# Kernel tuning notes

Hardware: AMD Instinct MI355X
Metric: run time of the kernel (lower is better)

The kernel has to match this reference:

```python
import jax, jax.numpy as jnp
import numpy as np

N, E, G, D = 100000, 400000, 4000, 128
AF, BF, L = 74, 12, 11  # atom/bond feat sizes; L = n_layers-1 GNN layers after GetContext


def _p(k, shape, fan):
    return jax.random.normal(k, shape, dtype=jnp.float32) * (fan ** -0.5)


def setup_inputs() -> dict:
    key = jax.random.key(0)
    ks = iter(jax.random.split(key, 32))
    z = lambda *s: jnp.zeros(s, jnp.float32)
    return dict(
        atom_feats=jax.random.normal(next(ks), (N, AF), jnp.float32),
        bond_feats=jax.random.normal(next(ks), (E, BF), jnp.float32),
        src=jax.random.randint(next(ks), (E,), 0, N, jnp.int32),
        dst=jax.random.randint(next(ks), (E,), 0, N, jnp.int32),
        node_graph_ids=jnp.sort(jax.random.randint(next(ks), (N,), 0, G, jnp.int32)),
        W_node=_p(next(ks), (AF, D), AF), b_node=z(D),
        W_edge1=_p(next(ks), (AF + BF, D), AF + BF), b_edge1=z(D),
        W_edge2=_p(next(ks), (2 * D, 1), 2 * D), b_edge2=z(1),
        W_et=_p(next(ks), (D, D), D), b_et=z(D),
        gru0_Wih=_p(next(ks), (3 * D, D), D), gru0_bih=z(3 * D),
        gru0_Whh=_p(next(ks), (3 * D, D), D), gru0_bhh=z(3 * D),
        Wpe=_p(next(ks), (L, 2 * D, 1), 2 * D), bpe=z(L, 1),
        Wpn=_p(next(ks), (L, D, D), D), bpn=z(L, D),
        gru_Wih=_p(next(ks), (L, 3 * D, D), D), gru_bih=z(L, 3 * D),
        gru_Whh=_p(next(ks), (L, 3 * D, D), D), gru_bhh=z(L, 3 * D),
        Wr1=_p(next(ks), (D, D), D), br1=z(D),
        Wr2=_p(next(ks), (D, D), D), br2=z(D),
    )


def leaky_relu(x):
    return jnp.where(x > 0, x, 0.01 * x)


def edge_softmax(logits, dst):
    # softmax of edge logits grouped by destination node (DGL edge_softmax)
    m = jax.ops.segment_max(logits, dst, num_segments=N)
    m = jnp.where(jnp.isfinite(m), m, 0.0)
    e = jnp.exp(logits - m[dst])
    s = jax.ops.segment_sum(e, dst, num_segments=N)
    return e / s[dst]


def gru_cell(x, h, Wih, bih, Whh, bhh):
    gi = x @ Wih.T + bih
    gh = h @ Whh.T + bhh
    ir, iz, ig = jnp.split(gi, 3, axis=-1)
    hr, hz, hg = jnp.split(gh, 3, axis=-1)
    r = jax.nn.sigmoid(ir + hr)
    z = jax.nn.sigmoid(iz + hz)
    n = jnp.tanh(ig + r * hg)
    return (1.0 - z) * n + z * h


def _attentive_fp(atom_feats, bond_feats, src, dst, node_graph_ids,
                  W_node, b_node, W_edge1, b_edge1, W_edge2, b_edge2,
                  W_et, b_et, gru0_Wih, gru0_bih, gru0_Whh, gru0_bhh,
                  Wpe, bpe, Wpn, bpn, gru_Wih, gru_bih, gru_Whh, gru_bhh,
                  Wr1, br1, Wr2, br2):
    # --- GetContext (dropout = identity at inference) ---
    hv_new = leaky_relu(atom_feats @ W_node + b_node)                       # [N,D]
    he1 = leaky_relu(jnp.concatenate([atom_feats[src], bond_feats], 1) @ W_edge1 + b_edge1)  # [E,D]
    logits = leaky_relu(jnp.concatenate([hv_new[dst], he1], 1) @ W_edge2 + b_edge2)          # [E,1]
    a = edge_softmax(logits, dst)
    c = jax.ops.segment_sum(a * (he1 @ W_et + b_et), dst, num_segments=N)   # [N,D]
    h = jax.nn.relu(gru_cell(jax.nn.elu(c), hv_new, gru0_Wih, gru0_bih, gru0_Whh, gru0_bhh))

    # --- 11 GNNLayers (AttentiveGRU2) via scan over stacked params ---
    def layer(h, p):
        Wpe_l, bpe_l, Wpn_l, bpn_l, Wih, bih, Whh, bhh = p
        lg = leaky_relu(jnp.concatenate([h[dst], h[src]], 1) @ Wpe_l + bpe_l)  # [E,1]
        a = edge_softmax(lg, dst)
        hp = h @ Wpn_l + bpn_l
        c = jax.ops.segment_sum(hp[src] * a, dst, num_segments=N)
        return jax.nn.relu(gru_cell(jax.nn.elu(c), h, Wih, bih, Whh, bhh)), None

    h, _ = jax.lax.scan(layer, h, (Wpe, bpe, Wpn, bpn, gru_Wih, gru_bih, gru_Whh, gru_bhh))

    # --- MLPNodeReadout, mode='mean' ---
    x = jax.nn.relu(h @ Wr1 + br1) @ Wr2 + br2
    sums = jax.ops.segment_sum(x, node_graph_ids, num_segments=G)
    counts = jax.ops.segment_sum(jnp.ones((N, 1), x.dtype), node_graph_ids, num_segments=G)
    return sums / jnp.maximum(counts, 1.0)                                  # [G,D]


def reference(atom_feats, bond_feats, src, dst, node_graph_ids,
              W_node, b_node, W_edge1, b_edge1, W_edge2, b_edge2,
              W_et, b_et, gru0_Wih, gru0_bih, gru0_Whh, gru0_bhh,
              Wpe, bpe, Wpn, bpn, gru_Wih, gru_bih, gru_Whh, gru_bhh,
              Wr1, br1, Wr2, br2):
    return _attentive_fp(atom_feats, bond_feats, src, dst, node_graph_ids,
                         W_node, b_node, W_edge1, b_edge1, W_edge2, b_edge2,
                         W_et, b_et, gru0_Wih, gru0_bih, gru0_Whh, gru0_bhh,
                         Wpe, bpe, Wpn, bpn, gru_Wih, gru_bih, gru_Whh, gru_bhh,
                         Wr1, br1, Wr2, br2)
```

## Files before the change

### kernel.cpp

```cpp
#include <hip/hip_runtime.h>
#include <cstdio>
#include <cstddef>

enum { ACT_NONE = 0, ACT_LEAKY = 1, ACT_RELU = 2 };

typedef __attribute__((ext_vector_type(8))) short short8v;
typedef __attribute__((ext_vector_type(4))) float f32x4;

__device__ __forceinline__ float leakyf(float x) { return x > 0.f ? x : 0.01f * x; }

__device__ __forceinline__ unsigned fenc(float f) {
    unsigned u = __float_as_uint(f);
    return (u & 0x80000000u) ? ~u : (u | 0x80000000u);
}
__device__ __forceinline__ float fdec(unsigned u) {
    return (u & 0x80000000u) ? __uint_as_float(u & 0x7FFFFFFFu) : __uint_as_float(~u);
}

__device__ __forceinline__ unsigned bf16rtn(float x) {
    unsigned u = __float_as_uint(x);
    return (u + 0x7FFFu + ((u >> 16) & 1u)) >> 16;
}
__device__ __forceinline__ void split8(float4 a, float4 b, short8v& hi, short8v& lo) {
    const float v[8] = {a.x, a.y, a.z, a.w, b.x, b.y, b.z, b.w};
#pragma unroll
    for (int i = 0; i < 8; i++) {
        const unsigned hb = bf16rtn(v[i]);
        const float r = v[i] - __uint_as_float(hb << 16);
        hi[i] = (short)hb;
        lo[i] = (short)bf16rtn(r);
    }
}

__global__ __launch_bounds__(256) void wsplit_k(
    const float* __restrict__ Wih, const float* __restrict__ Whh,
    unsigned short* __restrict__ whi, unsigned short* __restrict__ wlo)
{
    const int i4 = (blockIdx.x * 256 + threadIdx.x) * 4;
    if (i4 >= 98304) return;
    const float* src = (i4 < 49152) ? (Wih + i4) : (Whh + (i4 - 49152));
    const float4 v = *(const float4*)src;
    const float vv[4] = {v.x, v.y, v.z, v.w};
    unsigned short h4[4], l4[4];
#pragma unroll
    for (int i = 0; i < 4; i++) {
        const unsigned hb = bf16rtn(vv[i]);
        const float r = vv[i] - __uint_as_float(hb << 16);
        h4[i] = (unsigned short)hb;
        l4[i] = (unsigned short)bf16rtn(r);
    }
    *(ushort4*)&whi[i4] = make_ushort4(h4[0], h4[1], h4[2], h4[3]);
    *(ushort4*)&wlo[i4] = make_ushort4(l4[0], l4[1], l4[2], l4[3]);
}

__global__ __launch_bounds__(256) void wsplitT_k(
    const float* __restrict__ W,
    unsigned short* __restrict__ whi, unsigned short* __restrict__ wlo)
{
    const int idx = blockIdx.x * 256 + threadIdx.x;
    if (idx >= 16384) return;
    const int k = idx >> 7, col = idx & 127;
    const float v = W[idx];
    const unsigned hb = bf16rtn(v);
    const float r = v - __uint_as_float(hb << 16);
    whi[col * 128 + k] = (unsigned short)hb;
    wlo[col * 128 + k] = (unsigned short)bf16rtn(r);
}

__global__ __launch_bounds__(256) void wsplitT96_k(
    const float* __restrict__ W,
    unsigned short* __restrict__ whi, unsigned short* __restrict__ wlo, int K)
{
    const int idx = blockIdx.x * 256 + threadIdx.x;
    if (idx >= 12288) return;
    const int col = idx / 96, k = idx - col * 96;
    const float v = (k < K) ? W[(size_t)k * 128 + col] : 0.f;
    const unsigned hb = bf16rtn(v);
    const float r = v - __uint_as_float(hb << 16);
    whi[idx] = (unsigned short)hb;
    wlo[idx] = (unsigned short)bf16rtn(r);
}

__global__ __launch_bounds__(512) void gru_fused_mfma_k(
    const float* __restrict__ cbuf, const unsigned short* __restrict__ whi,
    const unsigned short* __restrict__ wlo, const float* __restrict__ bih,
    const float* __restrict__ bhh, float* __restrict__ h, int M)
{
    __shared__ short lhi[4][4][64][8];
    __shared__ short llo[4][4][64][8];
    const int t    = threadIdx.x;
    const int lane = t & 63;
    const int w    = t >> 6;
    const int rBase = blockIdx.x * 64;

    const int sRS = t >> 3, sQ = t & 7;
    const int sRow = rBase + sRS;
    const int sRT = sRS >> 4, sLrow = sRS & 15;

    auto stage = [&](const float* __restrict__ A, bool doElu) {
#pragma unroll
        for (int half = 0; half < 2; half++) {
            const int k0 = sQ * 16 + half * 8;
            const int kc = k0 >> 5;
            const int g  = (k0 & 31) >> 3;
            float4 f0 = make_float4(0.f, 0.f, 0.f, 0.f);
            float4 f1 = make_float4(0.f, 0.f, 0.f, 0.f);
            if (sRow < M) {
                f0 = *(const float4*)&A[(size_t)sRow * 128 + k0];
                f1 = *(const float4*)&A[(size_t)sRow * 128 + k0 + 4];
                if (doElu) {
                    f0.x = f0.x > 0.f ? f0.x : expm1f(f0.x);
                    f0.y = f0.y > 0.f ? f0.y : expm1f(f0.y);
                    f0.z = f0.z > 0.f ? f0.z : expm1f(f0.z);
                    f0.w = f0.w > 0.f ? f0.w : expm1f(f0.w);
                    f1.x = f1.x > 0.f ? f1.x : expm1f(f1.x);
                    f1.y = f1.y > 0.f ? f1.y : expm1f(f1.y);
                    f1.z = f1.z > 0.f ? f1.z : expm1f(f1.z);
                    f1.w = f1.w > 0.f ? f1.w : expm1f(f1.w);
                }
            }
            short8v h8, l8;
            split8(f0, f1, h8, l8);
            *(short8v*)&lhi[sRT][kc][sLrow + g * 16][0] = h8;
            *(short8v*)&llo[sRT][kc][sLrow + g * 16][0] = l8;
        }
    };

    f32x4 accr[4], accz[4], accig[4], acchg[4];
#pragma unroll
    for (int rt = 0; rt < 4; rt++) {
        accr[rt]  = (f32x4){0.f, 0.f, 0.f, 0.f};
        accz[rt]  = (f32x4){0.f, 0.f, 0.f, 0.f};
        accig[rt] = (f32x4){0.f, 0.f, 0.f, 0.f};
        acchg[rt] = (f32x4){0.f, 0.f, 0.f, 0.f};
    }

    const int cw   = w * 16 + (lane & 15);
    const int koff = (lane >> 4) * 8;

    stage(cbuf, true);
    __syncthreads();
#pragma unroll
    for (int kc = 0; kc < 4; kc++) {
        short8v bh[3], bl[3];
#pragma unroll
        for (int g = 0; g < 3; g++) {
            const size_t off = (size_t)(g * 128 + cw) * 128 + kc * 32 + koff;
            bh[g] = *(const short8v*)&whi[off];
            bl[g] = *(const short8v*)&wlo[off];
        }
#pragma unroll
        for (int rt = 0; rt < 4; rt++) {
            const short8v ah = *(const short8v*)&lhi[rt][kc][lane][0];
            const short8v al = *(const short8v*)&llo[rt][kc][lane][0];
            accr[rt]  = __builtin_amdgcn_mfma_f32_16x16x32_bf16(ah, bh[0], accr[rt], 0, 0, 0);
            accr[rt]  = __builtin_amdgcn_mfma_f32_16x16x32_bf16(al, bh[0], accr[rt], 0, 0, 0);
            accr[rt]  = __builtin_amdgcn_mfma_f32_16x16x32_bf16(ah, bl[0], accr[rt], 0, 0, 0);
            accz[rt]  = __builtin_amdgcn_mfma_f32_16x16x32_bf16(ah, bh[1], accz[rt], 0, 0, 0);
            accz[rt]  = __builtin_amdgcn_mfma_f32_16x16x32_bf16(al, bh[1], accz[rt], 0, 0, 0);
            accz[rt]  = __builtin_amdgcn_mfma_f32_16x16x32_bf16(ah, bl[1], accz[rt], 0, 0, 0);
            accig[rt] = __builtin_amdgcn_mfma_f32_16x16x32_bf16(ah, bh[2], accig[rt], 0, 0, 0);
            accig[rt] = __builtin_amdgcn_mfma_f32_16x16x32_bf16(al, bh[2], accig[rt], 0, 0, 0);
            accig[rt] = __builtin_amdgcn_mfma_f32_16x16x32_bf16(ah, bl[2], accig[rt], 0, 0, 0);
        }
    }
    __syncthreads();

    stage(h, false);
    __syncthreads();
#pragma unroll
    for (int kc = 0; kc < 4; kc++) {
        short8v bh[3], bl[3];
#pragma unroll
        for (int g = 0; g < 3; g++) {
            const size_t off = (size_t)(384 + g * 128 + cw) * 128 + kc * 32 + koff;
            bh[g] = *(const short8v*)&whi[off];
            bl[g] = *(const short8v*)&wlo[off];
        }
#pragma unroll
        for (int rt = 0; rt < 4; rt++) {
            const short8v ah = *(const short8v*)&lhi[rt][kc][lane][0];
            const short8v al = *(const short8v*)&llo[rt][kc][lane][0];
            accr[rt]  = __builtin_amdgcn_mfma_f32_16x16x32_bf16(ah, bh[0], accr[rt], 0, 0, 0);
            accr[rt]  = __builtin_amdgcn_mfma_f32_16x16x32_bf16(al, bh[0], accr[rt], 0, 0, 0);
            accr[rt]  = __builtin_amdgcn_mfma_f32_16x16x32_bf16(ah, bl[0], accr[rt], 0, 0, 0);
            accz[rt]  = __builtin_amdgcn_mfma_f32_16x16x32_bf16(ah, bh[1], accz[rt], 0, 0, 0);
            accz[rt]  = __builtin_amdgcn_mfma_f32_16x16x32_bf16(al, bh[1], accz[rt], 0, 0, 0);
            accz[rt]  = __builtin_amdgcn_mfma_f32_16x16x32_bf16(ah, bl[1], accz[rt], 0, 0, 0);
            acchg[rt] = __builtin_amdgcn_mfma_f32_16x16x32_bf16(ah, bh[2], acchg[rt], 0, 0, 0);
            acchg[rt] = __builtin_amdgcn_mfma_f32_16x16x32_bf16(al, bh[2], acchg[rt], 0, 0, 0);
            acchg[rt] = __builtin_amdgcn_mfma_f32_16x16x32_bf16(ah, bl[2], acchg[rt], 0, 0, 0);
        }
    }

    const float br_  = bih[cw] + bhh[cw];
    const float bz_  = bih[128 + cw] + bhh[128 + cw];
    const float big_ = bih[256 + cw];
    const float bhg_ = bhh[256 + cw];
#pragma unroll
    for (int rt = 0; rt < 4; rt++) {
        const int r0 = rBase + rt * 16 + ((lane >> 4) << 2);
#pragma unroll
        for (int i = 0; i < 4; i++) {
            const int row = r0 + i;
            if (row >= M) continue;
            const float hv = h[(size_t)row * 128 + cw];
            const float r  = 1.f / (1.f + expf(-(accr[rt][i] + br_)));
            const float z  = 1.f / (1.f + expf(-(accz[rt][i] + bz_)));
            const float nn = tanhf(accig[rt][i] + big_ + r * (acchg[rt][i] + bhg_));
            h[(size_t)row * 128 + cw] = fmaxf((1.f - z) * nn + z * hv, 0.f);
        }
    }
}

__global__ __launch_bounds__(512) void mfma128_k(
    const float* __restrict__ A, const unsigned short* __restrict__ whi,
    const unsigned short* __restrict__ wlo, const float* __restrict__ bias,
    float* __restrict__ C, int M, int actOut)
{
    __shared__ short lhi[4][4][64][8];
    __shared__ short llo[4][4][64][8];
    const int t    = threadIdx.x;
    const int lane = t & 63;
    const int w    = t >> 6;
    const int rBase = blockIdx.x * 64;

    {
        const int rS = t >> 3, q = t & 7;
        const int row = rBase + rS;
        const int rt = rS >> 4, lrow = rS & 15;
#pragma unroll
        for (int half = 0; half < 2; half++) {
            const int k0 = q * 16 + half * 8;
            const int kc = k0 >> 5;
            const int g  = (k0 & 31) >> 3;
            float4 f0 = make_float4(0.f, 0.f, 0.f, 0.f);
            float4 f1 = make_float4(0.f, 0.f, 0.f, 0.f);
            if (row < M) {
                f0 = *(const float4*)&A[(size_t)row * 128 + k0];
                f1 = *(const float4*)&A[(size_t)row * 128 + k0 + 4];
            }
            short8v h8, l8;
            split8(f0, f1, h8, l8);
            *(short8v*)&lhi[rt][kc][lrow + g * 16][0] = h8;
            *(short8v*)&llo[rt][kc][lrow + g * 16][0] = l8;
        }
    }
    __syncthreads();

    f32x4 acc[4];
#pragma unroll
    for (int rt = 0; rt < 4; rt++) acc[rt] = (f32x4){0.f, 0.f, 0.f, 0.f};

    const int cw   = w * 16 + (lane & 15);
    const int koff = (lane >> 4) * 8;

#pragma unroll
    for (int kc = 0; kc < 4; kc++) {
        const size_t off = (size_t)cw * 128 + kc * 32 + koff;
        const short8v bh = *(const short8v*)&whi[off];
        const short8v bl = *(const short8v*)&wlo[off];
#pragma unroll
        for (int rt = 0; rt < 4; rt++) {
            const short8v ah = *(const short8v*)&lhi[rt][kc][lane][0];
            const short8v al = *(const short8v*)&llo[rt][kc][lane][0];
            acc[rt] = __builtin_amdgcn_mfma_f32_16x16x32_bf16(ah, bh, acc[rt], 0, 0, 0);
            acc[rt] = __builtin_amdgcn_mfma_f32_16x16x32_bf16(al, bh, acc[rt], 0, 0, 0);
            acc[rt] = __builtin_amdgcn_mfma_f32_16x16x32_bf16(ah, bl, acc[rt], 0, 0, 0);
        }
    }

    const float b0 = bias[cw];
#pragma unroll
    for (int rt = 0; rt < 4; rt++) {
        const int r0 = rBase + rt * 16 + ((lane >> 4) << 2);
#pragma unroll
        for (int i = 0; i < 4; i++) {
            const int row = r0 + i;
            if (row >= M) continue;
            float v = acc[rt][i] + b0;
            if (actOut == ACT_LEAKY)      v = v > 0.f ? v : 0.01f * v;
            else if (actOut == ACT_RELU)  v = fmaxf(v, 0.f);
            C[(size_t)row * 128 + cw] = v;
        }
    }
}

__global__ __launch_bounds__(512) void mfma96_k(
    const float* __restrict__ A1, const float* __restrict__ A2,
    const int* __restrict__ idx,
    const unsigned short* __restrict__ whi, const unsigned short* __restrict__ wlo,
    const float* __restrict__ bias, float* __restrict__ C,
    int M, int K1, int actOut)
{
    __shared__ short lhi[4][3][64][8];
    __shared__ short llo[4][3][64][8];
    const int t    = threadIdx.x;
    const int lane = t & 63;
    const int w    = t >> 6;
    const int rBase = blockIdx.x * 64;

    {
        const int rS = t >> 3, q = t & 7;
        const int row = rBase + rS;
        const int rt = rS >> 4, lrow = rS & 15;
#pragma unroll
        for (int half = 0; half < 2; half++) {
            const int k0 = q * 16 + half * 8;
            if (k0 >= 96) continue;
            const int kc = k0 >> 5;
            const int g  = (k0 & 31) >> 3;
            float v[8] = {0.f, 0.f, 0.f, 0.f, 0.f, 0.f, 0.f, 0.f};
            if (row < M) {
                const int ar = idx ? idx[row] : row;
                const float* __restrict__ a1 = A1 + (size_t)ar * K1;
#pragma unroll
                for (int j = 0; j < 8; j++) {
                    const int k = k0 + j;
                    if (k < K1)                 v[j] = a1[k];
                    else if (A2 && k < K1 + 12) v[j] = A2[(size_t)row * 12 + (k - K1)];
                }
            }
            short8v h8, l8;
            split8(make_float4(v[0], v[1], v[2], v[3]),
                   make_float4(v[4], v[5], v[6], v[7]), h8, l8);
            *(short8v*)&lhi[rt][kc][lrow + g * 16][0] = h8;
            *(short8v*)&llo[rt][kc][lrow + g * 16][0] = l8;
        }
    }
    __syncthreads();

    f32x4 acc[4];
#pragma unroll
    for (int rt = 0; rt < 4; rt++) acc[rt] = (f32x4){0.f, 0.f, 0.f, 0.f};

    const int cw   = w * 16 + (lane & 15);
    const int koff = (lane >> 4) * 8;

#pragma unroll
    for (int kc = 0; kc < 3; kc++) {
        const size_t off = (size_t)cw * 96 + kc * 32 + koff;
        const short8v bh = *(const short8v*)&whi[off];
        const short8v bl = *(const short8v*)&wlo[off];
#pragma unroll
        for (int rt = 0; rt < 4; rt++) {
            const short8v ah = *(const short8v*)&lhi[rt][kc][lane][0];
            const short8v al = *(const short8v*)&llo[rt][kc][lane][0];
            acc[rt] = __builtin_amdgcn_mfma_f32_16x16x32_bf16(ah, bh, acc[rt], 0, 0, 0);
            acc[rt] = __builtin_amdgcn_mfma_f32_16x16x32_bf16(al, bh, acc[rt], 0, 0, 0);
            acc[rt] = __builtin_amdgcn_mfma_f32_16x16x32_bf16(ah, bl, acc[rt], 0, 0, 0);
        }
    }

    const float b0 = bias[cw];
#pragma unroll
    for (int rt = 0; rt < 4; rt++) {
        const int r0 = rBase + rt * 16 + ((lane >> 4) << 2);
#pragma unroll
        for (int i = 0; i < 4; i++) {
            const int row = r0 + i;
            if (row >= M) continue;
            float v = acc[rt][i] + b0;
            if (actOut == ACT_LEAKY)      v = v > 0.f ? v : 0.01f * v;
            else if (actOut == ACT_RELU)  v = fmaxf(v, 0.f);
            C[(size_t)row * 128 + cw] = v;
        }
    }
}

__global__ __launch_bounds__(256) void node_dots_k(
    const float* __restrict__ h, const float* __restrict__ wa,
    const float* __restrict__ wb, float* __restrict__ pd, float* __restrict__ ps, int n)
{
    const int i = blockIdx.x * 4 + (threadIdx.x >> 6);
    const int l = threadIdx.x & 63;
    if (i >= n) return;
    const float2 hv = *(const float2*)&h[(size_t)i * 128 + l * 2];
    float a = hv.x * wa[l * 2] + hv.y * wa[l * 2 + 1];
    float b = 0.f;
    if (wb) b = hv.x * wb[l * 2] + hv.y * wb[l * 2 + 1];
#pragma unroll
    for (int o = 32; o; o >>= 1) {
        a += __shfl_down(a, o, 64);
        b += __shfl_down(b, o, 64);
    }
    if (l == 0) {
        pd[i] = a;
        if (ps) ps[i] = b;
    }
}

__global__ __launch_bounds__(256) void edge_lgc_k(
    const float* __restrict__ pd, const float* __restrict__ pe,
    const float* __restrict__ b2, const int* __restrict__ dst,
    float* __restrict__ lg, unsigned* __restrict__ m_u, int E)
{
    const int e = blockIdx.x * blockDim.x + threadIdx.x;
    if (e >= E) return;
    const int d = dst[e];
    const float v = leakyf(pd[d] + pe[e] + b2[0]);
    lg[e] = v;
    atomicMax(&m_u[d], fenc(v));
}

__global__ __launch_bounds__(256) void edge_exp_k(
    float* __restrict__ lg, const unsigned* __restrict__ m_u,
    float* __restrict__ s, const int* __restrict__ dst, int E)
{
    const int e = blockIdx.x * blockDim.x + threadIdx.x;
    if (e >= E) return;
    const int d = dst[e];
    const float ex = expf(lg[e] - fdec(m_u[d]));
    lg[e] = ex;
    atomicAdd(&s[d], ex);
}

__global__ __launch_bounds__(256) void scatter_c_k(
    const float* __restrict__ rows,
    const float* __restrict__ ee, const float* __restrict__ s,
    const int* __restrict__ dst, float* __restrict__ c, int E)
{
    const long long gid = (long long)blockIdx.x * blockDim.x + threadIdx.x;
    const int e = (int)(gid >> 6);
    const int l = (int)(gid & 63);
    if (e >= E) return;
    const int d = dst[e];
    const float a = ee[e] / s[d];
    const float2 v = *(const float2*)&rows[(size_t)e * 128 + l * 2];
    atomicAdd(&c[(size_t)d * 128 + l * 2], a * v.x);
    atomicAdd(&c[(size_t)d * 128 + l * 2 + 1], a * v.y);
}

__global__ __launch_bounds__(256) void hist_k(
    const int* __restrict__ dst, unsigned* __restrict__ cnt, int E)
{
    const int e = blockIdx.x * blockDim.x + threadIdx.x;
    if (e < E) atomicAdd(&cnt[dst[e]], 1u);
}

__global__ __launch_bounds__(1024) void scan_k(
    const unsigned* __restrict__ cnt, int* __restrict__ rp, int N)
{
    __shared__ int wsum[16];
    __shared__ int carry;
    const int t = threadIdx.x, lane = t & 63, wid = t >> 6;
    if (t == 0) carry = 0;
    __syncthreads();
    for (int base = 0; base < N; base += 1024) {
        const int i = base + t;
        const int v = (i < N) ? (int)cnt[i] : 0;
        int x = v;
#pragma unroll
        for (int o = 1; o < 64; o <<= 1) {
            const int y = __shfl_up(x, o, 64);
            if (lane >= o) x += y;
        }
        if (lane == 63) wsum[wid] = x;
        __syncthreads();
        if (wid == 0) {
            const int wv = (lane < 16) ? wsum[lane] : 0;
            int wx = wv;
#pragma unroll
            for (int o = 1; o < 16; o <<= 1) {
                const int y = __shfl_up(wx, o, 64);
                if (lane >= o) wx += y;
            }
            if (lane < 16) wsum[lane] = wx - wv;
        }
        __syncthreads();
        const int excl = carry + wsum[wid] + x - v;
        if (i < N) rp[i] = excl;
        __syncthreads();
        if (t == 1023) carry = excl + v;
        __syncthreads();
    }
    if (t == 0) rp[N] = carry;
}

__global__ __launch_bounds__(256) void fill_csr_k(
    const int* __restrict__ dst, int* __restrict__ pos,
    int* __restrict__ eidx, int E)
{
    const int e = blockIdx.x * blockDim.x + threadIdx.x;
    if (e < E) {
        const int p = atomicAdd(&pos[dst[e]], 1);
        eidx[p] = e;
    }
}

__global__ __launch_bounds__(256) void layer_gather_k(
    const int* __restrict__ rp, const int* __restrict__ eidx,
    const int* __restrict__ src,
    const float* __restrict__ pd, const float* __restrict__ ps,
    const float* __restrict__ bpe,
    const float* __restrict__ hp, float* __restrict__ c, int N)
{
    const int d = blockIdx.x * 4 + (threadIdx.x >> 6);
    const int l = threadIdx.x & 63;
    if (d >= N) return;
    const int beg = rp[d], end = rp[d + 1];
    float acc0 = 0.f, acc1 = 0.f;
    if (beg < end) {
        const float pdd = pd[d];
        const float b   = bpe[0];
        float m = -3.4e38f;
        for (int e = beg + l; e < end; e += 64)
            m = fmaxf(m, leakyf(pdd + ps[src[eidx[e]]] + b));
#pragma unroll
        for (int o = 32; o; o >>= 1) m = fmaxf(m, __shfl_xor(m, o, 64));
        float s = 0.f;
        for (int e = beg + l; e < end; e += 64)
            s += expf(leakyf(pdd + ps[src[eidx[e]]] + b) - m);
#pragma unroll
        for (int o = 32; o; o >>= 1) s += __shfl_xor(s, o, 64);
        const float inv = 1.f / s;
        for (int e = beg; e < end; ++e) {
            const int sr = src[eidx[e]];
            const float a = expf(leakyf(pdd + ps[sr] + b) - m) * inv;
            const float2 v = *(const float2*)&hp[(size_t)sr * 128 + l * 2];
            acc0 = fmaf(a, v.x, acc0);
            acc1 = fmaf(a, v.y, acc1);
        }
    }
    *(float2*)&c[(size_t)d * 128 + l * 2] = make_float2(acc0, acc1);
}

__global__ __launch_bounds__(256) void readout_mean_k(
    const float* __restrict__ x, const int* __restrict__ grp,
    float* __restrict__ out, int G)
{
    const int g = blockIdx.x * 4 + (threadIdx.x >> 6);
    const int l = threadIdx.x & 63;
    if (g >= G) return;
    const int beg = grp[g], end = grp[g + 1];
    float s0 = 0.f, s1 = 0.f;
    for (int r = beg; r < end; ++r) {
        const float2 v = *(const float2*)&x[(size_t)r * 128 + l * 2];
        s0 += v.x;
        s1 += v.y;
    }
    const float inv = 1.f / fmaxf((float)(end - beg), 1.f);
    *(float2*)&out[(size_t)g * 128 + l * 2] = make_float2(s0 * inv, s1 * inv);
}

extern "C" void kernel_launch(void* const* d_in, const int* in_sizes, int n_in,
                              void* d_out, int out_size, void* d_ws, size_t ws_size,
                              hipStream_t stream)
{
    const float* atom   = (const float*)d_in[0];
    const float* bond   = (const float*)d_in[1];
    const int*   src    = (const int*)d_in[2];
    const int*   dst    = (const int*)d_in[3];
    const int*   ngid   = (const int*)d_in[4];
    const float* W_node = (const float*)d_in[5];
    const float* b_node = (const float*)d_in[6];
    const float* W_e1   = (const float*)d_in[7];
    const float* b_e1   = (const float*)d_in[8];
    const float* W_e2   = (const float*)d_in[9];
    const float* b_e2   = (const float*)d_in[10];
    const float* W_et   = (const float*)d_in[11];
    const float* b_et   = (const float*)d_in[12];
    const float* g0_Wih = (const float*)d_in[13];
    const float* g0_bih = (const float*)d_in[14];
    const float* g0_Whh = (const float*)d_in[15];
    const float* g0_bhh = (const float*)d_in[16];
    const float* Wpe    = (const float*)d_in[17];
    const float* bpe    = (const float*)d_in[18];
    const float* Wpn    = (const float*)d_in[19];
    const float* bpn    = (const float*)d_in[20];
    const float* gWih   = (const float*)d_in[21];
    const float* gbih   = (const float*)d_in[22];
    const float* gWhh   = (const float*)d_in[23];
    const float* gbhh   = (const float*)d_in[24];
    const float* Wr1    = (const float*)d_in[25];
    const float* br1    = (const float*)d_in[26];
    const float* Wr2    = (const float*)d_in[27];
    const float* br2    = (const float*)d_in[28];

    const int N = in_sizes[0] / 74;
    const int E = in_sizes[1] / 12;
    const int G = out_size / 128;
    const int L = in_sizes[18];

    char* w = (char*)d_ws;
    auto align256 = [](size_t b) { return (b + 255) & ~(size_t)255; };
    auto alloc = [&](size_t bytes) {
        void* p = (void*)w;
        w += align256(bytes);
        return p;
    };
    float*    h    = (float*)alloc((size_t)N * 128 * 4);
    float*    c    = (float*)alloc((size_t)N * 128 * 4);
    float*    hp   = (float*)alloc((size_t)N * 128 * 4);
    int*      rp   = (int*)alloc((size_t)(N + 1) * 4);
    int*      posb = (int*)alloc((size_t)N * 4);
    int*      eidx = (int*)alloc((size_t)E * 4);
    int*      grp  = (int*)alloc((size_t)(G + 1) * 4);
    unsigned short* gwHi  = (unsigned short*)alloc((size_t)12 * 98304 * 2);
    unsigned short* gwLo  = (unsigned short*)alloc((size_t)12 * 98304 * 2);
    unsigned short* wtHi  = (unsigned short*)alloc((size_t)14 * 16384 * 2);
    unsigned short* wtLo  = (unsigned short*)alloc((size_t)14 * 16384 * 2);
    unsigned short* w96Hi = (unsigned short*)alloc((size_t)2 * 12288 * 2);
    unsigned short* w96Lo = (unsigned short*)alloc((size_t)2 * 12288 * 2);
    float*    pd   = (float*)alloc((size_t)N * 4);
    float*    ps   = (float*)alloc((size_t)N * 4);
    unsigned* m_u  = (unsigned*)alloc((size_t)N * 4);
    float*    sden = (float*)alloc((size_t)N * 4);
    float*    pe   = (float*)alloc((size_t)E * 4);
    float*    lg   = (float*)alloc((size_t)E * 4);
    if ((size_t)(w - (char*)d_ws) > ws_size) {
        fprintf(stderr, "kernel_launch: ws too small: need %zu, have %zu\n",
                (size_t)(w - (char*)d_ws), ws_size);
        return;
    }
    float* out = (float*)d_out;

    const dim3 blk(256);
    auto g64 = [](int M) { return dim3((unsigned)((M + 63) / 64)); };
    const dim3 gEdge((unsigned)((E + 255) / 256));
    const dim3 gWave4N((unsigned)((N + 3) / 4));
    const int  Ecap = N;

    wsplit_k<<<dim3(96), blk, 0, stream>>>(g0_Wih, g0_Whh, gwHi, gwLo);
    for (int l = 0; l < L; ++l)
        wsplit_k<<<dim3(96), blk, 0, stream>>>(
            gWih + (size_t)l * 49152, gWhh + (size_t)l * 49152,
            gwHi + (size_t)(l + 1) * 98304, gwLo + (size_t)(l + 1) * 98304);
    for (int l = 0; l < L; ++l)
        wsplitT_k<<<dim3(64), blk, 0, stream>>>(
            Wpn + (size_t)l * 16384, wtHi + (size_t)l * 16384, wtLo + (size_t)l * 16384);
    wsplitT_k<<<dim3(64), blk, 0, stream>>>(W_et, wtHi + (size_t)11 * 16384, wtLo + (size_t)11 * 16384);
    wsplitT_k<<<dim3(64), blk, 0, stream>>>(Wr1,  wtHi + (size_t)12 * 16384, wtLo + (size_t)12 * 16384);
    wsplitT_k<<<dim3(64), blk, 0, stream>>>(Wr2,  wtHi + (size_t)13 * 16384, wtLo + (size_t)13 * 16384);
    wsplitT96_k<<<dim3(48), blk, 0, stream>>>(W_e1,   w96Hi,         w96Lo,         86);
    wsplitT96_k<<<dim3(48), blk, 0, stream>>>(W_node, w96Hi + 12288, w96Lo + 12288, 74);

    auto run_gru = [&](int slot, const float* bih, const float* bhh) {
        gru_fused_mfma_k<<<g64(N), dim3(512), 0, stream>>>(
            c, gwHi + (size_t)slot * 98304, gwLo + (size_t)slot * 98304, bih, bhh, h, N);
    };
    auto run_mfma128 = [&](const float* A, int slot, const float* bias,
                           float* C, int act) {
        mfma128_k<<<g64(N), dim3(512), 0, stream>>>(
            A, wtHi + (size_t)slot * 16384, wtLo + (size_t)slot * 16384, bias, C, N, act);
    };

    hipMemsetAsync(m_u, 0, (size_t)N * 4, stream);
    hist_k<<<gEdge, blk, 0, stream>>>(dst, m_u, E);
    scan_k<<<dim3(1), dim3(1024), 0, stream>>>(m_u, rp, N);
    hipMemcpyAsync(posb, rp, (size_t)N * 4, hipMemcpyDeviceToDevice, stream);
    fill_csr_k<<<gEdge, blk, 0, stream>>>(dst, posb, eidx, E);
    hipMemsetAsync(m_u, 0, (size_t)G * 4, stream);
    hist_k<<<dim3((unsigned)((N + 255) / 256)), blk, 0, stream>>>(ngid, m_u, N);
    scan_k<<<dim3(1), dim3(1024), 0, stream>>>(m_u, grp, G);

    mfma96_k<<<g64(N), dim3(512), 0, stream>>>(
        atom, nullptr, nullptr, w96Hi + 12288, w96Lo + 12288, b_node, h, N, 74, ACT_LEAKY);
    node_dots_k<<<gWave4N, blk, 0, stream>>>(h, W_e2, nullptr, pd, nullptr, N);
    for (int base = 0; base < E; base += Ecap) {
        const int ec = (E - base) < Ecap ? (E - base) : Ecap;
        mfma96_k<<<g64(ec), dim3(512), 0, stream>>>(
            atom, bond + (size_t)base * 12, src + base, w96Hi, w96Lo, b_e1,
            hp, ec, 74, ACT_LEAKY);
        node_dots_k<<<dim3((unsigned)((ec + 3) / 4)), blk, 0, stream>>>(
            hp, W_e2 + 128, nullptr, pe + base, nullptr, ec);
    }
    hipMemsetAsync(m_u, 0, (size_t)N * 4, stream);
    hipMemsetAsync(sden, 0, (size_t)N * 4, stream);
    edge_lgc_k<<<gEdge, blk, 0, stream>>>(pd, pe, b_e2, dst, lg, m_u, E);
    edge_exp_k<<<gEdge, blk, 0, stream>>>(lg, m_u, sden, dst, E);
    hipMemsetAsync(c, 0, (size_t)N * 128 * 4, stream);
    for (int base = 0; base < E; base += Ecap) {
        const int ec = (E - base) < Ecap ? (E - base) : Ecap;
        mfma96_k<<<g64(ec), dim3(512), 0, stream>>>(
            atom, bond + (size_t)base * 12, src + base, w96Hi, w96Lo, b_e1,
            hp, ec, 74, ACT_LEAKY);
        scatter_c_k<<<dim3((unsigned)(((long long)ec * 64 + 255) / 256)), blk, 0, stream>>>(
            hp, lg + base, sden, dst + base, c, ec);
    }
    run_mfma128(c, 11, b_et, c, ACT_NONE);
    run_gru(0, g0_bih, g0_bhh);

    for (int l = 0; l < L; ++l) {
        node_dots_k<<<gWave4N, blk, 0, stream>>>(
            h, Wpe + (size_t)l * 256, Wpe + (size_t)l * 256 + 128, pd, ps, N);
        run_mfma128(h, l, bpn + (size_t)l * 128, hp, ACT_NONE);
        layer_gather_k<<<gWave4N, blk, 0, stream>>>(
            rp, eidx, src, pd, ps, bpe + l, hp, c, N);
        run_gru(l + 1, gbih + (size_t)l * 384, gbhh + (size_t)l * 384);
    }

    run_mfma128(h, 12, br1, c, ACT_RELU);
    run_mfma128(c, 13, br2, hp, ACT_NONE);
    readout_mean_k<<<dim3((unsigned)((G + 3) / 4)), blk, 0, stream>>>(hp, grp, out, G);

    (void)n_in;
}
```

Measured before the change: 4.072 ms.

## Fuse node attention dot products into GEMM and GRU epilogues

The standalone node_dots_k kernel is removed. Its per-row dot products are computed inside the mfma96 and GRU epilogues using 16-lane shuffle reductions, with atomicAdd into zeroed pd/ps/pe buffers. The first edge pass no longer writes the hp intermediate, and the GRU kernel double-buffers its LDS staging so c and h are both staged before one barrier. This cuts a full reread of h or hp per layer and several launches, at the cost of extra memsets, atomics, doubled shared memory (which may lower occupancy), and summation-order changes.

```diff
diff --git a/kernel.cpp b/kernel.cpp
--- a/kernel.cpp
+++ b/kernel.cpp
@@ -84,10 +84,12 @@
 __global__ __launch_bounds__(512) void gru_fused_mfma_k(
     const float* __restrict__ cbuf, const unsigned short* __restrict__ whi,
     const unsigned short* __restrict__ wlo, const float* __restrict__ bih,
-    const float* __restrict__ bhh, float* __restrict__ h, int M)
-{
-    __shared__ short lhi[4][4][64][8];
-    __shared__ short llo[4][4][64][8];
+    const float* __restrict__ bhh, float* __restrict__ h,
+    const float* __restrict__ wa, const float* __restrict__ wb,
+    float* __restrict__ pd, float* __restrict__ ps, int M)
+{
+    __shared__ short lhi[2][4][4][64][8];
+    __shared__ short llo[2][4][4][64][8];
     const int t    = threadIdx.x;
     const int lane = t & 63;
     const int w    = t >> 6;
@@ -97,7 +99,7 @@
     const int sRow = rBase + sRS;
     const int sRT = sRS >> 4, sLrow = sRS & 15;
 
-    auto stage = [&](const float* __restrict__ A, bool doElu) {
+    auto stage = [&](int buf, const float* __restrict__ A, bool doElu) {
 #pragma unroll
         for (int half = 0; half < 2; half++) {
             const int k0 = sQ * 16 + half * 8;
@@ -121,8 +123,8 @@
             }
             short8v h8, l8;
             split8(f0, f1, h8, l8);
-            *(short8v*)&lhi[sRT][kc][sLrow + g * 16][0] = h8;
-            *(short8v*)&llo[sRT][kc][sLrow + g * 16][0] = l8;
+            *(short8v*)&lhi[buf][sRT][kc][sLrow + g * 16][0] = h8;
+            *(short8v*)&llo[buf][sRT][kc][sLrow + g * 16][0] = l8;
         }
     };
 
@@ -138,8 +140,10 @@
     const int cw   = w * 16 + (lane & 15);
     const int koff = (lane >> 4) * 8;
 
-    stage(cbuf, true);
+    stage(0, cbuf, true);
+    stage(1, h, false);
     __syncthreads();
+
 #pragma unroll
     for (int kc = 0; kc < 4; kc++) {
         short8v bh[3], bl[3];
@@ -151,8 +155,8 @@
         }
 #pragma unroll
         for (int rt = 0; rt < 4; rt++) {
-            const short8v ah = *(const short8v*)&lhi[rt][kc][lane][0];
-            const short8v al = *(const short8v*)&llo[rt][kc][lane][0];
+            const short8v ah = *(const short8v*)&lhi[0][rt][kc][lane][0];
+            const short8v al = *(const short8v*)&llo[0][rt][kc][lane][0];
             accr[rt]  = __builtin_amdgcn_mfma_f32_16x16x32_bf16(ah, bh[0], accr[rt], 0, 0, 0);
             accr[rt]  = __builtin_amdgcn_mfma_f32_16x16x32_bf16(al, bh[0], accr[rt], 0, 0, 0);
             accr[rt]  = __builtin_amdgcn_mfma_f32_16x16x32_bf16(ah, bl[0], accr[rt], 0, 0, 0);
@@ -164,10 +168,6 @@
             accig[rt] = __builtin_amdgcn_mfma_f32_16x16x32_bf16(ah, bl[2], accig[rt], 0, 0, 0);
         }
     }
-    __syncthreads();
-
-    stage(h, false);
-    __syncthreads();
 #pragma unroll
     for (int kc = 0; kc < 4; kc++) {
         short8v bh[3], bl[3];
@@ -179,8 +179,8 @@
         }
 #pragma unroll
         for (int rt = 0; rt < 4; rt++) {
-            const short8v ah = *(const short8v*)&lhi[rt][kc][lane][0];
-            const short8v al = *(const short8v*)&llo[rt][kc][lane][0];
+            const short8v ah = *(const short8v*)&lhi[1][rt][kc][lane][0];
+            const short8v al = *(const short8v*)&llo[1][rt][kc][lane][0];
             accr[rt]  = __builtin_amdgcn_mfma_f32_16x16x32_bf16(ah, bh[0], accr[rt], 0, 0, 0);
             accr[rt]  = __builtin_amdgcn_mfma_f32_16x16x32_bf16(al, bh[0], accr[rt], 0, 0, 0);
             accr[rt]  = __builtin_amdgcn_mfma_f32_16x16x32_bf16(ah, bl[0], accr[rt], 0, 0, 0);
@@ -197,18 +197,37 @@
     const float bz_  = bih[128 + cw] + bhh[128 + cw];
     const float big_ = bih[256 + cw];
     const float bhg_ = bhh[256 + cw];
+    const float wav = wa ? wa[cw] : 0.f;
+    const float wbv = wa ? wb[cw] : 0.f;
 #pragma unroll
     for (int rt = 0; rt < 4; rt++) {
         const int r0 = rBase + rt * 16 + ((lane >> 4) << 2);
 #pragma unroll
         for (int i = 0; i < 4; i++) {
             const int row = r0 + i;
-            if (row >= M) continue;
-            const float hv = h[(size_t)row * 128 + cw];
-            const float r  = 1.f / (1.f + expf(-(accr[rt][i] + br_)));
-            const float z  = 1.f / (1.f + expf(-(accz[rt][i] + bz_)));
-            const float nn = tanhf(accig[rt][i] + big_ + r * (acchg[rt][i] + bhg_));
-            h[(size_t)row * 128 + cw] = fmaxf((1.f - z) * nn + z * hv, 0.f);
+            const bool ok = (row < M);
+            float hnew = 0.f;
+            if (ok) {
+                const float hv = h[(size_t)row * 128 + cw];
+                const float r  = 1.f / (1.f + expf(-(accr[rt][i] + br_)));
+                const float z  = 1.f / (1.f + expf(-(accz[rt][i] + bz_)));
+                const float nn = tanhf(accig[rt][i] + big_ + r * (acchg[rt][i] + bhg_));
+                hnew = fmaxf((1.f - z) * nn + z * hv, 0.f);
+                h[(size_t)row * 128 + cw] = hnew;
+            }
+            if (wa) {
+                float dv = hnew * wav;
+                float sv = hnew * wbv;
+#pragma unroll
+                for (int o = 1; o < 16; o <<= 1) {
+                    dv += __shfl_xor(dv, o, 64);
+                    sv += __shfl_xor(sv, o, 64);
+                }
+                if (ok && (lane & 15) == 0) {
+                    atomicAdd(&pd[row], dv);
+                    atomicAdd(&ps[row], sv);
+                }
+            }
         }
     }
 }
@@ -291,7 +310,8 @@
     const int* __restrict__ idx,
     const unsigned short* __restrict__ whi, const unsigned short* __restrict__ wlo,
     const float* __restrict__ bias, float* __restrict__ C,
-    int M, int K1, int actOut)
+    const float* __restrict__ dotW, float* __restrict__ dotOut,
+    int writeC, int M, int K1, int actOut)
 {
     __shared__ short lhi[4][3][64][8];
     __shared__ short llo[4][3][64][8];
@@ -353,40 +373,25 @@
     }
 
     const float b0 = bias[cw];
+    const float dwv = dotOut ? dotW[cw] : 0.f;
 #pragma unroll
     for (int rt = 0; rt < 4; rt++) {
         const int r0 = rBase + rt * 16 + ((lane >> 4) << 2);
 #pragma unroll
         for (int i = 0; i < 4; i++) {
             const int row = r0 + i;
-            if (row >= M) continue;
+            const bool ok = (row < M);
             float v = acc[rt][i] + b0;
             if (actOut == ACT_LEAKY)      v = v > 0.f ? v : 0.01f * v;
             else if (actOut == ACT_RELU)  v = fmaxf(v, 0.f);
-            C[(size_t)row * 128 + cw] = v;
-        }
-    }
-}
-
-__global__ __launch_bounds__(256) void node_dots_k(
-    const float* __restrict__ h, const float* __restrict__ wa,
-    const float* __restrict__ wb, float* __restrict__ pd, float* __restrict__ ps, int n)
-{
-    const int i = blockIdx.x * 4 + (threadIdx.x >> 6);
-    const int l = threadIdx.x & 63;
-    if (i >= n) return;
-    const float2 hv = *(const float2*)&h[(size_t)i * 128 + l * 2];
-    float a = hv.x * wa[l * 2] + hv.y * wa[l * 2 + 1];
-    float b = 0.f;
-    if (wb) b = hv.x * wb[l * 2] + hv.y * wb[l * 2 + 1];
-#pragma unroll
-    for (int o = 32; o; o >>= 1) {
-        a += __shfl_down(a, o, 64);
-        b += __shfl_down(b, o, 64);
-    }
-    if (l == 0) {
-        pd[i] = a;
-        if (ps) ps[i] = b;
+            if (ok && writeC) C[(size_t)row * 128 + cw] = v;
+            if (dotOut) {
+                float dv = ok ? v * dwv : 0.f;
+#pragma unroll
+                for (int o = 1; o < 16; o <<= 1) dv += __shfl_xor(dv, o, 64);
+                if (ok && (lane & 15) == 0) atomicAdd(&dotOut[row], dv);
+            }
+        }
     }
 }
 
@@ -618,7 +623,6 @@
     const dim3 blk(256);
     auto g64 = [](int M) { return dim3((unsigned)((M + 63) / 64)); };
     const dim3 gEdge((unsigned)((E + 255) / 256));
-    const dim3 gWave4N((unsigned)((N + 3) / 4));
     const int  Ecap = N;
 
     wsplit_k<<<dim3(96), blk, 0, stream>>>(g0_Wih, g0_Whh, gwHi, gwLo);
@@ -635,9 +639,15 @@
     wsplitT96_k<<<dim3(48), blk, 0, stream>>>(W_e1,   w96Hi,         w96Lo,         86);
     wsplitT96_k<<<dim3(48), blk, 0, stream>>>(W_node, w96Hi + 12288, w96Lo + 12288, 74);
 
-    auto run_gru = [&](int slot, const float* bih, const float* bhh) {
+    auto run_gru = [&](int slot, const float* bih, const float* bhh,
+                       const float* wav, const float* wbv) {
+        if (wav) {
+            hipMemsetAsync(pd, 0, (size_t)N * 4, stream);
+            hipMemsetAsync(ps, 0, (size_t)N * 4, stream);
+        }
         gru_fused_mfma_k<<<g64(N), dim3(512), 0, stream>>>(
-            c, gwHi + (size_t)slot * 98304, gwLo + (size_t)slot * 98304, bih, bhh, h, N);
+            c, gwHi + (size_t)slot * 98304, gwLo + (size_t)slot * 98304,
+            bih, bhh, h, wav, wbv, pd, ps, N);
     };
     auto run_mfma128 = [&](const float* A, int slot, const float* bias,
                            float* C, int act) {
@@ -654,16 +664,16 @@
     hist_k<<<dim3((unsigned)((N + 255) / 256)), blk, 0, stream>>>(ngid, m_u, N);
     scan_k<<<dim3(1), dim3(1024), 0, stream>>>(m_u, grp, G);
 
+    hipMemsetAsync(pd, 0, (size_t)N * 4, stream);
     mfma96_k<<<g64(N), dim3(512), 0, stream>>>(
-        atom, nullptr, nullptr, w96Hi + 12288, w96Lo + 12288, b_node, h, N, 74, ACT_LEAKY);
-    node_dots_k<<<gWave4N, blk, 0, stream>>>(h, W_e2, nullptr, pd, nullptr, N);
+        atom, nullptr, nullptr, w96Hi + 12288, w96Lo + 12288, b_node, h,
+        W_e2, pd, 1, N, 74, ACT_LEAKY);
+    hipMemsetAsync(pe, 0, (size_t)E * 4, stream);
     for (int base = 0; base < E; base += Ecap) {
         const int ec = (E - base) < Ecap ? (E - base) : Ecap;
         mfma96_k<<<g64(ec), dim3(512), 0, stream>>>(
             atom, bond + (size_t)base * 12, src + base, w96Hi, w96Lo, b_e1,
-            hp, ec, 74, ACT_LEAKY);
-        node_dots_k<<<dim3((unsigned)((ec + 3) / 4)), blk, 0, stream>>>(
-            hp, W_e2 + 128, nullptr, pe + base, nullptr, ec);
+            nullptr, W_e2 + 128, pe + base, 0, ec, 74, ACT_LEAKY);
     }
     hipMemsetAsync(m_u, 0, (size_t)N * 4, stream);
     hipMemsetAsync(sden, 0, (size_t)N * 4, stream);
@@ -674,20 +684,21 @@
         const int ec = (E - base) < Ecap ? (E - base) : Ecap;
         mfma96_k<<<g64(ec), dim3(512), 0, stream>>>(
             atom, bond + (size_t)base * 12, src + base, w96Hi, w96Lo, b_e1,
-            hp, ec, 74, ACT_LEAKY);
+            hp, nullptr, nullptr, 1, ec, 74, ACT_LEAKY);
         scatter_c_k<<<dim3((unsigned)(((long long)ec * 64 + 255) / 256)), blk, 0, stream>>>(
             hp, lg + base, sden, dst + base, c, ec);
     }
     run_mfma128(c, 11, b_et, c, ACT_NONE);
-    run_gru(0, g0_bih, g0_bhh);
+    run_gru(0, g0_bih, g0_bhh, Wpe, Wpe + 128);
 
     for (int l = 0; l < L; ++l) {
-        node_dots_k<<<gWave4N, blk, 0, stream>>>(
-            h, Wpe + (size_t)l * 256, Wpe + (size_t)l * 256 + 128, pd, ps, N);
         run_mfma128(h, l, bpn + (size_t)l * 128, hp, ACT_NONE);
-        layer_gather_k<<<gWave4N, blk, 0, stream>>>(
+        layer_gather_k<<<dim3((unsigned)((N + 3) / 4)), blk, 0, stream>>>(
             rp, eidx, src, pd, ps, bpe + l, hp, c, N);
-        run_gru(l + 1, gbih + (size_t)l * 384, gbhh + (size_t)l * 384);
+        const bool more = (l + 1 < L);
+        run_gru(l + 1, gbih + (size_t)l * 384, gbhh + (size_t)l * 384,
+                more ? (Wpe + (size_t)(l + 1) * 256) : nullptr,
+                more ? (Wpe + (size_t)(l + 1) * 256 + 128) : nullptr);
     }
 
     run_mfma128(h, 12, br1, c, ACT_RELU);
```

Result: slower. 4.198 ms (+3.1%).
